# Optimization experiments

Hardware: AMD Instinct MI355X
Metric: run time of the kernel (lower is better)

The kernel has to match this reference:

```python
import jax, jax.numpy as jnp
import numpy as np

KERNEL = 5
DILATIONS = (3, 1)
N_HEADS = 8
LN_EPS = 1e-5


def unfold1d(x, kernel, dilation, pad):
    # x: (N, H, S) -> (N, H, S, kernel) dilated sliding windows (same length)
    xp = jnp.pad(x, ((0, 0), (0, 0), (pad, pad)))
    S = x.shape[-1]
    idx = jnp.arange(S)[:, None] + jnp.arange(kernel)[None, :] * dilation  # (S, K)
    return xp[:, :, idx]  # (N, H, S, K)


def dilated_mha(q, k, v, Ws, bs, Wo, bo):
    # q,k,v: (B, S, D); Ws: (2, split, split); Wo: (D, D)
    B, S, D = q.shape
    ndil = len(DILATIONS)
    hpd = N_HEADS // ndil            # heads per dilation
    dk = D // N_HEADS
    split = D // ndil
    scale = dk ** (-0.5)
    outs, probs = [], []
    for i, dil in enumerate(DILATIONS):
        pad = dil * (KERNEL - 1) // 2
        sl = slice(i * split, (i + 1) * split)
        qi = q[..., sl] @ Ws[i].T + bs[i]
        ki = k[..., sl] @ Ws[i].T + bs[i]
        vi = v[..., sl] @ Ws[i].T + bs[i]
        # (B,S,hpd,dk) -> (B,dk,hpd,S), matching torch transpose(1,2).permute(0,3,1,2)
        to4 = lambda x: jnp.transpose(x.reshape(B, S, hpd, dk), (0, 3, 2, 1))
        qi4, ki4, vi4 = to4(qi), to4(ki), to4(vi)
        # unfold then reinterpret (B*dk,hpd,...) as (B*hpd,dk,...) exactly as torch .reshape does
        kp = unfold1d(ki4.reshape(B * dk, hpd, S), KERNEL, dil, pad).reshape(B * hpd, dk, S, KERNEL)
        vp = unfold1d(vi4.reshape(B * dk, hpd, S), KERNEL, dil, pad).reshape(B * hpd, dk, S, KERNEL)
        qr = qi4.reshape(B * hpd, dk, S)
        scores = jnp.einsum('nds,ndsk->nsk', qr, kp) * scale   # (B*hpd, S, K)
        p = jax.nn.softmax(scores, axis=-1)
        out = jnp.einsum('nsk,ndsk->nds', p, vp)               # (B*hpd, dk, S)
        out = jnp.transpose(out.reshape(B, hpd, dk, S), (0, 3, 1, 2)).reshape(B, S, split)
        outs.append(out)
        probs.append(p.reshape(B, hpd, S, KERNEL))
    o = jnp.concatenate(outs, axis=-1) @ Wo.T + bo
    return o, jnp.concatenate(probs, axis=1)


def layer_norm(x, g, b):
    mu = jnp.mean(x, axis=-1, keepdims=True)
    var = jnp.mean((x - mu) ** 2, axis=-1, keepdims=True)
    return (x - mu) * jax.lax.rsqrt(var + LN_EPS) * g + b


def setup_inputs() -> dict:
    key = jax.random.key(0)
    ks = jax.random.split(key, 6)
    B, S, D = 32, 2048, 256
    split = D // 2
    q_emb = jax.random.normal(ks[0], (B, S, D), dtype=jnp.float32)
    s_emb = jax.random.normal(ks[1], (B, S, D), dtype=jnp.float32)
    lens = jax.random.randint(ks[2], (B,), 5, S, dtype=jnp.int32)
    W_lin = jax.random.normal(ks[3], (3, 2, split, split), dtype=jnp.float32) * (split ** -0.5)
    b_lin = jnp.zeros((3, 2, split), dtype=jnp.float32)
    W_out = jax.random.normal(ks[4], (3, D, D), dtype=jnp.float32) * (D ** -0.5)
    b_out = jnp.zeros((3, D), dtype=jnp.float32)
    ln_g = jnp.ones((3, D), dtype=jnp.float32)
    ln_b = jnp.zeros((3, D), dtype=jnp.float32)
    return {"q_emb": q_emb, "s_emb": s_emb, "lens": lens, "W_lin": W_lin,
            "b_lin": b_lin, "W_out": W_out, "b_out": b_out, "ln_g": ln_g, "ln_b": ln_b}


def reference(q_emb, s_emb, lens, W_lin, b_lin, W_out, b_out, ln_g, ln_b):
    # CASTransformer.forward, shortcut=True path, eval mode (dropout=id, mask unused)
    a1, _ = dilated_mha(q_emb, q_emb, q_emb, W_lin[0], b_lin[0], W_out[0], b_out[0])
    hq = layer_norm(q_emb + a1, ln_g[0], ln_b[0])
    a2, q_scores = dilated_mha(s_emb, s_emb, s_emb, W_lin[1], b_lin[1], W_out[1], b_out[1])
    hs = layer_norm(s_emb + a2, ln_g[1], ln_b[1])
    a3, _ = dilated_mha(hq, hq, hs, W_lin[2], b_lin[2], W_out[2], b_out[2])
    z = layer_norm(hq + a3, ln_g[2], ln_b[2])
    return z, q_scores
```

## Files before the change

### kernel.cpp

```cpp
#include <hip/hip_runtime.h>
#include <hip/hip_bf16.h>

typedef __bf16 bf16x8 __attribute__((ext_vector_type(8)));
typedef float  f32x4  __attribute__((ext_vector_type(4)));
typedef unsigned int u32;
typedef u32 u32x4 __attribute__((ext_vector_type(4)));
typedef unsigned short ushort_t;

__device__ inline float bf2f(ushort_t h) {
    union { u32 u; float f; } v; v.u = ((u32)h) << 16; return v.f;
}
__device__ inline ushort_t f2bf(float f) {
    union { float f; u32 u; } v; v.f = f;
    u32 u = v.u;
    return (ushort_t)((u + 0x7fffu + ((u >> 16) & 1u)) >> 16);
}
__device__ inline bf16x8 load_bf8(const ushort_t* p) {
    u32x4 u = *reinterpret_cast<const u32x4*>(p);
    return __builtin_bit_cast(bf16x8, u);
}
__device__ inline bf16x8 load8_in(const void* base, size_t idx, int f32flag) {
    if (!f32flag) return load_bf8((const ushort_t*)base + idx);
    const float* pf = (const float*)base + idx;
    f32x4 a = *reinterpret_cast<const f32x4*>(pf);
    f32x4 b = *reinterpret_cast<const f32x4*>(pf + 4);
    bf16x8 r;
#pragma unroll
    for (int j = 0; j < 4; ++j) { r[j] = (__bf16)a[j]; r[4 + j] = (__bf16)b[j]; }
    return r;
}
__device__ inline float ld_in(const void* base, size_t idx, int f32flag) {
    return f32flag ? ((const float*)base)[idx] : bf2f(((const ushort_t*)base)[idx]);
}

__device__ inline int pofs(int row, int ch) { return row * 256 + (ch ^ ((row & 15) << 3)); }
__device__ inline int tofs(int tr, int ch) { return tr * 256 + (ch ^ (((tr + 8) & 15) << 3)); }

__global__ __launch_bounds__(256) void detect_kernel(const u32* __restrict__ d, int n,
                                                     int* __restrict__ flag) {
    const int t = threadIdx.x;
    int cn = 0, co = 0;
    for (int i = t; i < n; i += 256) {
        const u32 w = d[i];
        const u32 e  = (w >> 7) & 0xFF;
        const u32 fe = (w >> 23) & 0xFF;
        cn += (e >= 100 && e <= 135) ? 1 : 0;
        co += (((w & 0xFFFFu) == 0u) && fe >= 100 && fe <= 140) ? 1 : 0;
    }
    __shared__ int sn[256], so[256];
    sn[t] = cn; so[t] = co; __syncthreads();
    for (int o = 128; o; o >>= 1) {
        if (t < o) { sn[t] += sn[t + o]; so[t] += so[t + o]; }
        __syncthreads();
    }
    if (t == 0) {
        const int CN = sn[0], CO = so[0];
        const int is_f32 = (2 * CN < n) && ((2 * CO > n) || (20 * CN > n));
        *flag = is_f32 ? 1 : 0;
    }
}

__device__ inline int f_of(const int* flags, int i) { return i < 0 ? 0 : flags[i]; }
__device__ inline int out_f32(const int* flags) {
    return flags[0] | flags[1] | flags[3] | flags[4] | flags[5] | flags[6] | flags[7] | flags[8];
}

__global__ __launch_bounds__(256, 4) void proj_kernel(
    const void* __restrict__ X, int xi,
    const void* __restrict__ W, size_t lw,
    const void* __restrict__ Bv, size_t lb,
    ushort_t* __restrict__ Y, const int* __restrict__ flags)
{
    __shared__ ushort_t tile[64 * 256];
    const int xf  = f_of(flags, xi);
    const int wf  = flags[3], bfl = flags[4];
    const int tid = threadIdx.x;
    const int m0  = blockIdx.x * 64;

#pragma unroll
    for (int i = 0; i < 8; ++i) {
        const int c = tid + 256 * i;
        const int row = c >> 5, cc = c & 31;
        bf16x8 v = load8_in(X, (size_t)(m0 + row) * 256 + cc * 8, xf);
        *reinterpret_cast<u32x4*>(&tile[pofs(row, cc * 8)]) = __builtin_bit_cast(u32x4, v);
    }
    __syncthreads();

    const int wave = tid >> 6, lane = tid & 63;
    const int dil  = wave >> 1;
    const int n_off = (wave & 1) * 64;
    const int l15  = lane & 15, quad = lane >> 4;

    f32x4 acc[4][4] = {};
    for (int kc = 0; kc < 4; ++kc) {
        bf16x8 a[4], b[4];
#pragma unroll
        for (int mt = 0; mt < 4; ++mt)
            a[mt] = load_bf8(&tile[pofs(mt * 16 + l15, dil * 128 + kc * 32 + quad * 8)]);
#pragma unroll
        for (int nt = 0; nt < 4; ++nt)
            b[nt] = load8_in(W, lw + (size_t)dil * 16384 +
                             (size_t)(n_off + nt * 16 + l15) * 128 + kc * 32 + quad * 8, wf);
#pragma unroll
        for (int mt = 0; mt < 4; ++mt)
#pragma unroll
            for (int nt = 0; nt < 4; ++nt)
                acc[mt][nt] = __builtin_amdgcn_mfma_f32_16x16x32_bf16(a[mt], b[nt], acc[mt][nt], 0, 0, 0);
    }
    __syncthreads();

#pragma unroll
    for (int nt = 0; nt < 4; ++nt) {
        const int ncol = n_off + nt * 16 + l15;
        const float bias = ld_in(Bv, lb + dil * 128 + ncol, bfl);
#pragma unroll
        for (int mt = 0; mt < 4; ++mt)
#pragma unroll
            for (int r = 0; r < 4; ++r) {
                const int row = mt * 16 + quad * 4 + r;
                tile[pofs(row, dil * 128 + ncol)] = f2bf(acc[mt][nt][r] + bias);
            }
    }
    __syncthreads();

#pragma unroll
    for (int i = 0; i < 8; ++i) {
        const int c = tid + 256 * i;
        const int row = c >> 5, cc = c & 31;
        *reinterpret_cast<u32x4*>(Y + (size_t)(m0 + row) * 256 + cc * 8) =
            *reinterpret_cast<const u32x4*>(&tile[row * 256 + cc * 8]);
    }
}

__global__ __launch_bounds__(256, 4) void fused_attn_oln_kernel(
    const ushort_t* __restrict__ P, const ushort_t* __restrict__ V,
    const void* __restrict__ R, int ri,
    const void* __restrict__ W, size_t lw,
    const void* __restrict__ Bv, size_t lb,
    const void* __restrict__ G, const void* __restrict__ Bt, size_t lg,
    void* __restrict__ H, int h_out,
    void* __restrict__ probs_base,
    const int* __restrict__ flags)
{
    __shared__ ushort_t tile[80 * 256];
    float (*lsum)[64] = (float (*)[64])(&tile[0]);
    float (*lsq)[64]  = (float (*)[64])(&tile[1024]);

    const int wf = flags[5], bvf = flags[6], gf = flags[7], btf = flags[8];
    const int rf = f_of(flags, ri);
    const int og = out_f32(flags);
    const int of = h_out ? og : 0;

    const int tid  = threadIdx.x;
    const int wave = tid >> 6, lane = tid & 63;
    const int l15  = lane & 15, quad = lane >> 4;
    const int m0   = blockIdx.x * 64;
    const int bb   = m0 >> 11;
    const int s0   = m0 & 2047;
    const size_t rowbase = (size_t)bb * 2048;
    const float scale = 0.17677669529663687f;

#pragma unroll
    for (int i = 0; i < 10; ++i) {
        const int c = tid + 256 * i;
        const int tr = c >> 5, cc = c & 31;
        int s = s0 - 8 + tr; s = s < 0 ? 0 : (s > 2047 ? 2047 : s);
        *reinterpret_cast<u32x4*>(&tile[tr * 256 + cc * 8]) =
            *reinterpret_cast<const u32x4*>(P + (rowbase + s) * 256 + cc * 8);
    }
    __syncthreads();

    const int r = lane, g = wave;
    const int s = s0 + r;

    float p2[2][5];
#pragma unroll
    for (int it = 0; it < 2; ++it) {
        const int dil  = it;
        const int dila = dil ? 1 : 3;
        const int ch0  = dil * 128 + g * 8;

        float qv[4][8];
#pragma unroll
        for (int h = 0; h < 4; ++h) {
            bf16x8 t = load_bf8(&tile[tofs(8 + r, ch0 + h * 32)]);
#pragma unroll
            for (int j = 0; j < 8; ++j) qv[h][j] = (float)t[j];
        }
        float sc[5];
#pragma unroll
        for (int kk = 0; kk < 5; ++kk) {
            const int sp = s + (kk - 2) * dila;
            float a = 0.f;
            if (sp >= 0 && sp < 2048) {
                const int tr2 = 8 + r + (kk - 2) * dila;
#pragma unroll
                for (int h = 0; h < 4; ++h) {
                    bf16x8 t = load_bf8(&tile[tofs(tr2, ch0 + h * 32)]);
#pragma unroll
                    for (int j = 0; j < 8; ++j) a += qv[h][j] * (float)t[j];
                }
                a *= scale;
            }
            sc[kk] = a;
        }
        float mx = sc[0];
#pragma unroll
        for (int kk = 1; kk < 5; ++kk) mx = fmaxf(mx, sc[kk]);
        float sum = 0.f;
#pragma unroll
        for (int kk = 0; kk < 5; ++kk) { p2[it][kk] = __expf(sc[kk] - mx); sum += p2[it][kk]; }
        const float inv = 1.f / sum;
#pragma unroll
        for (int kk = 0; kk < 5; ++kk) p2[it][kk] *= inv;

        if (probs_base != nullptr) {
            const size_t pb = 16777216 + ((size_t)((bb * 8 + dil * 4 + g) * 2048 + s)) * 5;
            if (og) {
                float* pp = (float*)probs_base;
#pragma unroll
                for (int kk = 0; kk < 5; ++kk) pp[pb + kk] = p2[it][kk];
            } else {
                ushort_t* pp = (ushort_t*)probs_base;
#pragma unroll
                for (int kk = 0; kk < 5; ++kk) pp[pb + kk] = f2bf(p2[it][kk]);
            }
        }
    }

    if (V != P) {
        __syncthreads();
#pragma unroll
        for (int i = 0; i < 10; ++i) {
            const int c = tid + 256 * i;
            const int tr = c >> 5, cc = c & 31;
            int s2 = s0 - 8 + tr; s2 = s2 < 0 ? 0 : (s2 > 2047 ? 2047 : s2);
            *reinterpret_cast<u32x4*>(&tile[tr * 256 + cc * 8]) =
                *reinterpret_cast<const u32x4*>(V + (rowbase + s2) * 256 + cc * 8);
        }
        __syncthreads();
    }

    u32x4 wpk[2][4];
#pragma unroll
    for (int it = 0; it < 2; ++it) {
        const int dil  = it;
        const int dila = dil ? 1 : 3;
        const int ch0  = dil * 128 + g * 8;
        float o[4][8] = {};
#pragma unroll
        for (int kk = 0; kk < 5; ++kk) {
            const int sp = s + (kk - 2) * dila;
            if (sp < 0 || sp >= 2048) continue;
            const int tr2 = 8 + r + (kk - 2) * dila;
#pragma unroll
            for (int h = 0; h < 4; ++h) {
                bf16x8 t = load_bf8(&tile[tofs(tr2, ch0 + h * 32)]);
#pragma unroll
                for (int j = 0; j < 8; ++j) o[h][j] += p2[it][kk] * (float)t[j];
            }
        }
#pragma unroll
        for (int c = 0; c < 4; ++c) {
            u32x4 w;
#pragma unroll
            for (int t4 = 0; t4 < 4; ++t4) {
                const int d2a = c * 8 + t4 * 2, d2b = d2a + 1;
                const u32 lo = f2bf(o[d2a & 3][d2a >> 2]);
                const u32 hi = f2bf(o[d2b & 3][d2b >> 2]);
                w[t4] = lo | (hi << 16);
            }
            wpk[it][c] = w;
        }
    }
    __syncthreads();

#pragma unroll
    for (int it = 0; it < 2; ++it)
#pragma unroll
        for (int c = 0; c < 4; ++c)
            *reinterpret_cast<u32x4*>(&tile[tofs(8 + r, it * 128 + g * 32 + c * 8)]) = wpk[it][c];
    __syncthreads();

    const int n_off = wave * 64;

    f32x4 acc[4][4] = {};
    for (int kc = 0; kc < 8; ++kc) {
        bf16x8 a[4], b[4];
#pragma unroll
        for (int mt = 0; mt < 4; ++mt)
            a[mt] = load_bf8(&tile[tofs(8 + mt * 16 + l15, kc * 32 + quad * 8)]);
#pragma unroll
        for (int nt = 0; nt < 4; ++nt)
            b[nt] = load8_in(W, lw + (size_t)(n_off + nt * 16 + l15) * 256 + kc * 32 + quad * 8, wf);
#pragma unroll
        for (int mt = 0; mt < 4; ++mt)
#pragma unroll
            for (int nt = 0; nt < 4; ++nt)
                acc[mt][nt] = __builtin_amdgcn_mfma_f32_16x16x32_bf16(a[mt], b[nt], acc[mt][nt], 0, 0, 0);
    }

    float bias[4];
#pragma unroll
    for (int nt = 0; nt < 4; ++nt) bias[nt] = ld_in(Bv, lb + n_off + nt * 16 + l15, bvf);

    float psum[4][4] = {}, psq[4][4] = {};
#pragma unroll
    for (int mt = 0; mt < 4; ++mt) {
#pragma unroll
        for (int rr = 0; rr < 4; ++rr) {
            const size_t rrow = (size_t)(m0 + mt * 16 + quad * 4 + rr) * 256 + l15;
#pragma unroll
            for (int nt = 0; nt < 4; ++nt) {
                float v = acc[mt][nt][rr] + bias[nt] + ld_in(R, rrow + n_off + nt * 16, rf);
                acc[mt][nt][rr] = v;
                psum[mt][rr] += v;
                psq[mt][rr]  += v * v;
            }
        }
    }
#pragma unroll
    for (int off = 1; off <= 8; off <<= 1) {
#pragma unroll
        for (int mt = 0; mt < 4; ++mt)
#pragma unroll
            for (int rr = 0; rr < 4; ++rr) {
                psum[mt][rr] += __shfl_xor(psum[mt][rr], off);
                psq[mt][rr]  += __shfl_xor(psq[mt][rr],  off);
            }
    }
    if (l15 == 0) {
#pragma unroll
        for (int mt = 0; mt < 4; ++mt)
#pragma unroll
            for (int rr = 0; rr < 4; ++rr) {
                const int row = mt * 16 + quad * 4 + rr;
                lsum[wave][row] = psum[mt][rr];
                lsq[wave][row]  = psq[mt][rr];
            }
    }
    __syncthreads();

    float gl[4], blv[4];
#pragma unroll
    for (int nt = 0; nt < 4; ++nt) {
        gl[nt]  = ld_in(G,  lg + n_off + nt * 16 + l15, gf);
        blv[nt] = ld_in(Bt, lg + n_off + nt * 16 + l15, btf);
    }
#pragma unroll
    for (int mt = 0; mt < 4; ++mt) {
#pragma unroll
        for (int rr = 0; rr < 4; ++rr) {
            const int row = mt * 16 + quad * 4 + rr;
            const float sm = lsum[0][row] + lsum[1][row] + lsum[2][row] + lsum[3][row];
            const float q2 = lsq[0][row]  + lsq[1][row]  + lsq[2][row]  + lsq[3][row];
            const float mu  = sm * (1.f / 256.f);
            const float var = q2 * (1.f / 256.f) - mu * mu;
            const float rs  = rsqrtf(var + 1e-5f);
            const size_t hrow = (size_t)(m0 + row) * 256 + l15;
#pragma unroll
            for (int nt = 0; nt < 4; ++nt) {
                const float hv = (acc[mt][nt][rr] - mu) * rs * gl[nt] + blv[nt];
                if (of) ((float*)H)[hrow + n_off + nt * 16] = hv;
                else    ((ushort_t*)H)[hrow + n_off + nt * 16] = f2bf(hv);
            }
        }
    }
}

extern "C" void kernel_launch(void* const* d_in, const int* in_sizes, int n_in,
                              void* d_out, int out_size, void* d_ws, size_t ws_size,
                              hipStream_t stream) {
    const void* q_emb = d_in[0];
    const void* s_emb = d_in[1];
    const void* W_lin = d_in[3];
    const void* b_lin = d_in[4];
    const void* W_out = d_in[5];
    const void* b_out = d_in[6];
    const void* ln_g  = d_in[7];
    const void* ln_b  = d_in[8];

    const size_t SLOT = 16777216;
    int*      flags = (int*)d_ws;
    ushort_t* SA = (ushort_t*)((char*)d_ws + 256);
    ushort_t* SB = SA + SLOT;
    ushort_t* SC = SA + 2 * SLOT;

    const dim3 blk(256);
    detect_kernel<<<1, blk, 0, stream>>>((const u32*)q_emb, 16384, flags + 0);
    detect_kernel<<<1, blk, 0, stream>>>((const u32*)s_emb, 16384, flags + 1);
    detect_kernel<<<1, blk, 0, stream>>>((const u32*)W_lin, 16384, flags + 3);
    detect_kernel<<<1, blk, 0, stream>>>((const u32*)b_lin,   384, flags + 4);
    detect_kernel<<<1, blk, 0, stream>>>((const u32*)W_out, 16384, flags + 5);
    detect_kernel<<<1, blk, 0, stream>>>((const u32*)b_out,   384, flags + 6);
    detect_kernel<<<1, blk, 0, stream>>>((const u32*)ln_g,    384, flags + 7);
    detect_kernel<<<1, blk, 0, stream>>>((const u32*)ln_b,    384, flags + 8);

    proj_kernel<<<1024, blk, 0, stream>>>(q_emb, 0, W_lin, 0, b_lin, 0, SC, flags);
    fused_attn_oln_kernel<<<1024, blk, 0, stream>>>(SC, SC, q_emb, 0,
        W_out, 0, b_out, 0, ln_g, ln_b, 0, SA, 0, nullptr, flags);
    proj_kernel<<<1024, blk, 0, stream>>>(s_emb, 1, W_lin, 32768, b_lin, 256, SC, flags);
    fused_attn_oln_kernel<<<1024, blk, 0, stream>>>(SC, SC, s_emb, 1,
        W_out, 65536, b_out, 256, ln_g, ln_b, 256, SB, 0, d_out, flags);
    proj_kernel<<<1024, blk, 0, stream>>>(SA, -1, W_lin, 65536, b_lin, 512, SC, flags);
    proj_kernel<<<1024, blk, 0, stream>>>(SB, -1, W_lin, 65536, b_lin, 512, SB, flags);
    fused_attn_oln_kernel<<<1024, blk, 0, stream>>>(SC, SB, SA, -1,
        W_out, 131072, b_out, 512, ln_g, ln_b, 512, d_out, 1, nullptr, flags);
}
```

Before: 621.8 us.

## Fuse third-layer projections into attention epilogues and batch detect/proj launches

Merges the eight dtype-detect launches into one 8-block kernel. Runs the first two input projections in a single 2048-block launch. Folds the stage-3 linear projection of hq and hs into the epilogue of the preceding attention+LN kernels, so the hq/hs round trip through global memory and two separate projection launches go away. The fp32 output store is staged through LDS for vectorized writes. The cost is heavier epilogues that add extra MFMA work and LDS syncs per block, plus a fourth workspace slot, with a fallback path when the workspace is too small.

```diff
diff --git a/kernel.cpp b/kernel.cpp
--- a/kernel.cpp
+++ b/kernel.cpp
@@ -36,8 +36,23 @@
 __device__ inline int pofs(int row, int ch) { return row * 256 + (ch ^ ((row & 15) << 3)); }
 __device__ inline int tofs(int tr, int ch) { return tr * 256 + (ch ^ (((tr + 8) & 15) << 3)); }
 
-__global__ __launch_bounds__(256) void detect_kernel(const u32* __restrict__ d, int n,
-                                                     int* __restrict__ flag) {
+__device__ inline int f_of(const int* flags, int i) { return i < 0 ? 0 : flags[i]; }
+__device__ inline int out_f32(const int* flags) {
+    return flags[0] | flags[1] | flags[3] | flags[4] | flags[5] | flags[6] | flags[7] | flags[8];
+}
+
+__global__ __launch_bounds__(256) void detect_all(
+    const u32* a0, const u32* a1, const u32* a2, const u32* a3,
+    const u32* a4, const u32* a5, const u32* a6, const u32* a7,
+    int* __restrict__ flags)
+{
+    const u32* arrs[8] = {a0, a1, a2, a3, a4, a5, a6, a7};
+    const int  ns[8]   = {16384, 16384, 16384, 384, 16384, 384, 384, 384};
+    const int  fi[8]   = {0, 1, 3, 4, 5, 6, 7, 8};
+    const int  b = blockIdx.x;
+    const u32* d = arrs[b];
+    const int  n = ns[b];
+
     const int t = threadIdx.x;
     int cn = 0, co = 0;
     for (int i = t; i < n; i += 256) {
@@ -56,26 +71,27 @@
     if (t == 0) {
         const int CN = sn[0], CO = so[0];
         const int is_f32 = (2 * CN < n) && ((2 * CO > n) || (20 * CN > n));
-        *flag = is_f32 ? 1 : 0;
-    }
-}
-
-__device__ inline int f_of(const int* flags, int i) { return i < 0 ? 0 : flags[i]; }
-__device__ inline int out_f32(const int* flags) {
-    return flags[0] | flags[1] | flags[3] | flags[4] | flags[5] | flags[6] | flags[7] | flags[8];
-}
-
-__global__ __launch_bounds__(256, 4) void proj_kernel(
-    const void* __restrict__ X, int xi,
-    const void* __restrict__ W, size_t lw,
-    const void* __restrict__ Bv, size_t lb,
-    ushort_t* __restrict__ Y, const int* __restrict__ flags)
+        flags[fi[b]] = is_f32 ? 1 : 0;
+    }
+}
+
+__global__ __launch_bounds__(256, 4) void proj2_kernel(
+    const void* X0, int xi0, size_t lw0, size_t lb0, ushort_t* __restrict__ Y0,
+    const void* X1, int xi1, size_t lw1, size_t lb1, ushort_t* __restrict__ Y1,
+    const void* __restrict__ W, const void* __restrict__ Bv, const int* __restrict__ flags)
 {
-    __shared__ ushort_t tile[64 * 256];
+    __shared__ __align__(16) ushort_t tile[64 * 256];
+    const int half = blockIdx.x >> 10;
+    const void* X = half ? X1 : X0;
+    const int   xi = half ? xi1 : xi0;
+    const size_t lw = half ? lw1 : lw0;
+    const size_t lb = half ? lb1 : lb0;
+    ushort_t* Y = half ? Y1 : Y0;
+
     const int xf  = f_of(flags, xi);
     const int wf  = flags[3], bfl = flags[4];
     const int tid = threadIdx.x;
-    const int m0  = blockIdx.x * 64;
+    const int m0  = (blockIdx.x & 1023) * 64;
 
 #pragma unroll
     for (int i = 0; i < 8; ++i) {
@@ -140,13 +156,17 @@
     const void* __restrict__ G, const void* __restrict__ Bt, size_t lg,
     void* __restrict__ H, int h_out,
     void* __restrict__ probs_base,
+    const void* __restrict__ Wl, size_t lwl,
+    const void* __restrict__ bl, size_t lbl,
+    ushort_t* __restrict__ Yp,
     const int* __restrict__ flags)
 {
-    __shared__ ushort_t tile[80 * 256];
+    __shared__ __align__(16) ushort_t tile[80 * 256];
     float (*lsum)[64] = (float (*)[64])(&tile[0]);
     float (*lsq)[64]  = (float (*)[64])(&tile[1024]);
 
     const int wf = flags[5], bvf = flags[6], gf = flags[7], btf = flags[8];
+    const int wlf = flags[3], blf = flags[4];
     const int rf = f_of(flags, ri);
     const int og = out_f32(flags);
     const int of = h_out ? og : 0;
@@ -357,13 +377,117 @@
             const float mu  = sm * (1.f / 256.f);
             const float var = q2 * (1.f / 256.f) - mu * mu;
             const float rs  = rsqrtf(var + 1e-5f);
-            const size_t hrow = (size_t)(m0 + row) * 256 + l15;
-#pragma unroll
-            for (int nt = 0; nt < 4; ++nt) {
-                const float hv = (acc[mt][nt][rr] - mu) * rs * gl[nt] + blv[nt];
-                if (of) ((float*)H)[hrow + n_off + nt * 16] = hv;
-                else    ((ushort_t*)H)[hrow + n_off + nt * 16] = f2bf(hv);
-            }
+#pragma unroll
+            for (int nt = 0; nt < 4; ++nt)
+                acc[mt][nt][rr] = (acc[mt][nt][rr] - mu) * rs * gl[nt] + blv[nt];
+        }
+    }
+    __syncthreads();
+
+    if (Yp != nullptr) {
+#pragma unroll
+        for (int mt = 0; mt < 4; ++mt)
+#pragma unroll
+            for (int rr = 0; rr < 4; ++rr) {
+                const int row = mt * 16 + quad * 4 + rr;
+#pragma unroll
+                for (int nt = 0; nt < 4; ++nt)
+                    tile[pofs(row, n_off + nt * 16 + l15)] = f2bf(acc[mt][nt][rr]);
+            }
+        __syncthreads();
+
+        if (H != nullptr) {
+#pragma unroll
+            for (int i = 0; i < 8; ++i) {
+                const int c = tid + 256 * i;
+                const int row = c >> 5, cc = c & 31;
+                const int sc8 = (cc * 8) ^ ((row & 15) << 3);
+                *reinterpret_cast<u32x4*>((ushort_t*)H + (size_t)(m0 + row) * 256 + cc * 8) =
+                    *reinterpret_cast<const u32x4*>(&tile[row * 256 + sc8]);
+            }
+        }
+        const int dil2 = wave >> 1;
+        const int n2   = (wave & 1) * 64;
+        f32x4 pacc[4][4] = {};
+        for (int kc = 0; kc < 4; ++kc) {
+            bf16x8 a2[4], b2[4];
+#pragma unroll
+            for (int mt = 0; mt < 4; ++mt)
+                a2[mt] = load_bf8(&tile[pofs(mt * 16 + l15, dil2 * 128 + kc * 32 + quad * 8)]);
+#pragma unroll
+            for (int nt = 0; nt < 4; ++nt)
+                b2[nt] = load8_in(Wl, lwl + (size_t)dil2 * 16384 +
+                                  (size_t)(n2 + nt * 16 + l15) * 128 + kc * 32 + quad * 8, wlf);
+#pragma unroll
+            for (int mt = 0; mt < 4; ++mt)
+#pragma unroll
+                for (int nt = 0; nt < 4; ++nt)
+                    pacc[mt][nt] = __builtin_amdgcn_mfma_f32_16x16x32_bf16(a2[mt], b2[nt], pacc[mt][nt], 0, 0, 0);
+        }
+        __syncthreads();
+
+#pragma unroll
+        for (int nt = 0; nt < 4; ++nt) {
+            const int ncol = n2 + nt * 16 + l15;
+            const float pb = ld_in(bl, lbl + dil2 * 128 + ncol, blf);
+#pragma unroll
+            for (int mt = 0; mt < 4; ++mt)
+#pragma unroll
+                for (int r2 = 0; r2 < 4; ++r2)
+                    tile[pofs(mt * 16 + quad * 4 + r2, dil2 * 128 + ncol)] = f2bf(pacc[mt][nt][r2] + pb);
+        }
+        __syncthreads();
+
+#pragma unroll
+        for (int i = 0; i < 8; ++i) {
+            const int c = tid + 256 * i;
+            const int row = c >> 5, cc = c & 31;
+            *reinterpret_cast<u32x4*>(Yp + (size_t)(m0 + row) * 256 + cc * 8) =
+                *reinterpret_cast<const u32x4*>(&tile[row * 256 + cc * 8]);
+        }
+    } else if (of) {
+        float* tf = (float*)tile;
+#pragma unroll
+        for (int hh = 0; hh < 2; ++hh) {
+#pragma unroll
+            for (int mh = 0; mh < 2; ++mh) {
+                const int mt = 2 * hh + mh;
+#pragma unroll
+                for (int rr = 0; rr < 4; ++rr) {
+                    const int lrow = mh * 16 + quad * 4 + rr;
+#pragma unroll
+                    for (int nt = 0; nt < 4; ++nt)
+                        tf[lrow * 256 + n_off + nt * 16 + l15] = acc[mt][nt][rr];
+                }
+            }
+            __syncthreads();
+#pragma unroll
+            for (int i = 0; i < 8; ++i) {
+                const int c = tid + 256 * i;
+                const int row = c >> 6, cc = c & 63;
+                *reinterpret_cast<f32x4*>((float*)H + (size_t)(m0 + hh * 32 + row) * 256 + cc * 4) =
+                    *reinterpret_cast<const f32x4*>(&tf[row * 256 + cc * 4]);
+            }
+            __syncthreads();
+        }
+    } else {
+#pragma unroll
+        for (int mt = 0; mt < 4; ++mt)
+#pragma unroll
+            for (int rr = 0; rr < 4; ++rr) {
+                const int row = mt * 16 + quad * 4 + rr;
+#pragma unroll
+                for (int nt = 0; nt < 4; ++nt)
+                    tile[pofs(row, n_off + nt * 16 + l15)] = f2bf(acc[mt][nt][rr]);
+            }
+        __syncthreads();
+#pragma unroll
+        for (int i = 0; i < 8; ++i) {
+            const int c = tid + 256 * i;
+            const int row = c >> 5, cc = c & 31;
+            const int sc8 = (cc * 8) ^ ((row & 15) << 3);
+            *reinterpret_cast<u32x4*>((ushort_t*)H + (size_t)(m0 + row) * 256 + cc * 8) =
+                *reinterpret_cast<const u32x4*>(&tile[row * 256 + sc8]);
         }
     }
 }
@@ -382,28 +506,45 @@
 
     const size_t SLOT = 16777216;
     int*      flags = (int*)d_ws;
-    ushort_t* SA = (ushort_t*)((char*)d_ws + 256);
-    ushort_t* SB = SA + SLOT;
-    ushort_t* SC = SA + 2 * SLOT;
+    ushort_t* S1 = (ushort_t*)((char*)d_ws + 256);
+    ushort_t* S2 = S1 + SLOT;
+    ushort_t* S3 = S1 + 2 * SLOT;
+    ushort_t* S4 = S1 + 3 * SLOT;
+    const size_t need4 = 256 + 4 * SLOT * sizeof(ushort_t);
 
     const dim3 blk(256);
-    detect_kernel<<<1, blk, 0, stream>>>((const u32*)q_emb, 16384, flags + 0);
-    detect_kernel<<<1, blk, 0, stream>>>((const u32*)s_emb, 16384, flags + 1);
-    detect_kernel<<<1, blk, 0, stream>>>((const u32*)W_lin, 16384, flags + 3);
-    detect_kernel<<<1, blk, 0, stream>>>((const u32*)b_lin,   384, flags + 4);
-    detect_kernel<<<1, blk, 0, stream>>>((const u32*)W_out, 16384, flags + 5);
-    detect_kernel<<<1, blk, 0, stream>>>((const u32*)b_out,   384, flags + 6);
-    detect_kernel<<<1, blk, 0, stream>>>((const u32*)ln_g,    384, flags + 7);
-    detect_kernel<<<1, blk, 0, stream>>>((const u32*)ln_b,    384, flags + 8);
-
-    proj_kernel<<<1024, blk, 0, stream>>>(q_emb, 0, W_lin, 0, b_lin, 0, SC, flags);
-    fused_attn_oln_kernel<<<1024, blk, 0, stream>>>(SC, SC, q_emb, 0,
-        W_out, 0, b_out, 0, ln_g, ln_b, 0, SA, 0, nullptr, flags);
-    proj_kernel<<<1024, blk, 0, stream>>>(s_emb, 1, W_lin, 32768, b_lin, 256, SC, flags);
-    fused_attn_oln_kernel<<<1024, blk, 0, stream>>>(SC, SC, s_emb, 1,
-        W_out, 65536, b_out, 256, ln_g, ln_b, 256, SB, 0, d_out, flags);
-    proj_kernel<<<1024, blk, 0, stream>>>(SA, -1, W_lin, 65536, b_lin, 512, SC, flags);
-    proj_kernel<<<1024, blk, 0, stream>>>(SB, -1, W_lin, 65536, b_lin, 512, SB, flags);
-    fused_attn_oln_kernel<<<1024, blk, 0, stream>>>(SC, SB, SA, -1,
-        W_out, 131072, b_out, 512, ln_g, ln_b, 512, d_out, 1, nullptr, flags);
-}
+    detect_all<<<8, blk, 0, stream>>>((const u32*)q_emb, (const u32*)s_emb, (const u32*)W_lin,
+        (const u32*)b_lin, (const u32*)W_out, (const u32*)b_out,
+        (const u32*)ln_g, (const u32*)ln_b, flags);
+
+    if (ws_size >= need4) {
+        proj2_kernel<<<2048, blk, 0, stream>>>(q_emb, 0, 0, 0, S1,
+                                               s_emb, 1, 32768, 256, S2,
+                                               W_lin, b_lin, flags);
+        fused_attn_oln_kernel<<<1024, blk, 0, stream>>>(S1, S1, q_emb, 0,
+            W_out, 0, b_out, 0, ln_g, ln_b, 0, S3, 0, nullptr,
+            W_lin, 65536, b_lin, 512, S4, flags);
+        fused_attn_oln_kernel<<<1024, blk, 0, stream>>>(S2, S2, s_emb, 1,
+            W_out, 65536, b_out, 256, ln_g, ln_b, 256, nullptr, 0, d_out,
+            W_lin, 65536, b_lin, 512, S1, flags);
+        fused_attn_oln_kernel<<<1024, blk, 0, stream>>>(S4, S1, S3, -1,
+            W_out, 131072, b_out, 512, ln_g, ln_b, 512, d_out, 1, nullptr,
+            W_lin, 0, b_lin, 0, nullptr, flags);
+    } else {
+        proj2_kernel<<<1024, blk, 0, stream>>>(q_emb, 0, 0, 0, S1,
+                                               q_emb, 0, 0, 0, S1, W_lin, b_lin, flags);
+        fused_attn_oln_kernel<<<1024, blk, 0, stream>>>(S1, S1, q_emb, 0,
+            W_out, 0, b_out, 0, ln_g, ln_b, 0, S2, 0, nullptr,
+            W_lin, 0, b_lin, 0, nullptr, flags);
+        proj2_kernel<<<1024, blk, 0, stream>>>(s_emb, 1, 32768, 256, S1,
+                                               s_emb, 1, 32768, 256, S1, W_lin, b_lin, flags);
+        fused_attn_oln_kernel<<<1024, blk, 0, stream>>>(S1, S1, s_emb, 1,
+            W_out, 65536, b_out, 256, ln_g, ln_b, 256, S3, 0, d_out,
+            W_lin, 0, b_lin, 0, nullptr, flags);
+        proj2_kernel<<<2048, blk, 0, stream>>>(S2, -1, 65536, 512, S1,
+                                               S3, -1, 65536, 512, S3, W_lin, b_lin, flags);
+        fused_attn_oln_kernel<<<1024, blk, 0, stream>>>(S1, S3, S2, -1,
+            W_out, 131072, b_out, 512, ln_g, ln_b, 512, d_out, 1, nullptr,
+            W_lin, 0, b_lin, 0, nullptr, flags);
+    }
+}
```

After: 678.4 us. 9.1% more time.
